# Kernel tuning notes

Measured on AMD Instinct MI355X. Metric: run time of the kernel, lower is better.

The kernel has to match this reference:

```python
import jax, jax.numpy as jnp
import numpy as np

B, TY, TX, TT, H, VS, VT = 32, 64, 64, 64, 512, 32000, 32000


def setup_inputs() -> dict:
    key = jax.random.key(0)
    ks = jax.random.split(key, 12)
    s = 0.05  # weight scale for numerical sanity
    return {
        "y_hidden": jax.random.normal(ks[0], (B, TY, H), jnp.float32),
        "y_hidden_null": jax.random.normal(ks[1], (1, H), jnp.float32),
        "target_state": jax.random.normal(ks[2], (B, TT, H), jnp.float32),
        "W_em": jax.random.normal(ks[3], (H, H), jnp.float32) * s,
        "b_em": jnp.zeros((H,), jnp.float32),
        "W_sv": jax.random.normal(ks[4], (H, VS), jnp.float32) * s,
        "b_sv": jnp.zeros((VS,), jnp.float32),
        "W_tv": jax.random.normal(ks[5], (H, VT), jnp.float32) * s,
        "b_tv": jnp.zeros((VT,), jnp.float32),
        "sources": jax.random.randint(ks[6], (B, TX), 0, VS, jnp.int32),
        "targets": jax.random.randint(ks[7], (B, TT), 0, VT, jnp.int32),
        "target_lengths": jax.random.randint(ks[8], (B,), 1, TT + 1, jnp.int32),
    }


def reference(y_hidden, y_hidden_null, target_state, W_em, b_em, W_sv, b_sv,
              W_tv, b_tv, sources, targets, target_lengths):
    # ---- emission (get_emission) ----
    ts = jnp.tanh(y_hidden @ W_em + b_em)            # (B, Ty, H)
    tsn = jnp.tanh(y_hidden_null @ W_em + b_em)      # (1, H)
    em_sm = jax.nn.softmax(ts @ W_sv + b_sv, axis=-1)        # (B, Ty, Vs)
    null_sm = jax.nn.softmax(tsn @ W_sv + b_sv, axis=-1)     # (1, Vs)
    # vectorized replacement of tf.map_fn + tf.gather: per-batch gather of source token columns
    em_g = jnp.take_along_axis(em_sm, sources[:, None, :], axis=-1)  # (B, Ty, Tx)
    null_g = null_sm[0][sources]                                     # (B, Tx)
    null_tiled = jnp.broadcast_to(null_g[:, None, :], (sources.shape[0], ts.shape[1], sources.shape[1]))
    emission_prob = jnp.concatenate([em_g, null_tiled], axis=1)      # (B, 2*Ty, Tx)

    # ---- reconstruction (get_target); keep_prob = 1 so dropout is identity ----
    tgt_sm = jax.nn.softmax(target_state @ W_tv + b_tv, axis=-1)     # (B, Tt, Vt)
    target_predicted = jnp.argmax(tgt_sm, axis=-1)                   # (B, Tt)
    # gather[t, targets[t]] then * eye then reduce_sum == diagonal pick: prob of own token
    target_prob = jnp.take_along_axis(tgt_sm, targets[:, :, None].astype(jnp.int32), axis=-1)[..., 0]  # (B, Tt)
    Tt = targets.shape[1]
    target_mask = (jnp.arange(Tt)[None, :] < target_lengths[:, None]).astype(target_prob.dtype)
    reconstruction_expectation = target_prob * target_mask
    reconstruction_expectation_log = jnp.log(target_prob) * target_mask
    return emission_prob, reconstruction_expectation, reconstruction_expectation_log, target_predicted
```

## Files before the change

### kernel.cpp

```cpp
#include <hip/hip_runtime.h>
#include <math.h>

#define H 512
#define V 32000
#define NVB 250

typedef unsigned short ushort_t;
typedef __attribute__((ext_vector_type(8))) short short8;
typedef __attribute__((ext_vector_type(4))) float f32x4;

__device__ __forceinline__ unsigned short f2bf(float x) {
    unsigned int u; __builtin_memcpy(&u, &x, 4);
    unsigned int r = (u + 0x7fffu + ((u >> 16) & 1u)) >> 16;
    return (unsigned short)r;
}
__device__ __forceinline__ float bfu2f(unsigned short h) {
    unsigned int u = ((unsigned int)h) << 16;
    float f; __builtin_memcpy(&f, &u, 4);
    return f;
}

__device__ __forceinline__ void t2_insert(float& m1, int& c1, float& m2, int& c2,
                                          float v, int idx) {
    if (v > m1 || (v == m1 && idx < c1)) { m2 = m1; c2 = c1; m1 = v; c1 = idx; }
    else if (v > m2 || (v == m2 && idx < c2)) { m2 = v; c2 = idx; }
}

__device__ __forceinline__ void gl16(const void* g, void* l) {
    __builtin_amdgcn_global_load_lds(
        (const __attribute__((address_space(1))) void*)g,
        (__attribute__((address_space(3))) void*)l,
        16, 0, 0);
}

__global__ __launch_bounds__(256) void k_emstate(
    const float* __restrict__ y_hidden, const float* __restrict__ y_null,
    const float* __restrict__ W, const float* __restrict__ bias,
    float* __restrict__ ts)
{
    const int NR = 2049;
    __shared__ float As[16][64];
    __shared__ float Bs[16][64];
    int rb = blockIdx.y, cb = blockIdx.x;
    int row0 = rb * 64, col0 = cb * 64;
    int tid = threadIdx.x;
    int tr = tid >> 4, tc = tid & 15;
    float acc[4][4] = {};
    for (int k0 = 0; k0 < H; k0 += 16) {
        {
            int r = tid >> 2;
            int kk = (tid & 3) << 2;
            int row = row0 + r;
            float4 v = make_float4(0.f, 0.f, 0.f, 0.f);
            if (row < 2048)       v = *(const float4*)&y_hidden[row * H + k0 + kk];
            else if (row == 2048) v = *(const float4*)&y_null[k0 + kk];
            As[kk + 0][r] = v.x; As[kk + 1][r] = v.y;
            As[kk + 2][r] = v.z; As[kk + 3][r] = v.w;
            int bk = tid >> 4, bc = (tid & 15) << 2;
            *(float4*)&Bs[bk][bc] = *(const float4*)&W[(k0 + bk) * H + col0 + bc];
        }
        __syncthreads();
#pragma unroll
        for (int kk = 0; kk < 16; ++kk) {
            float4 a = *(float4*)&As[kk][tr * 4];
            float4 b = *(float4*)&Bs[kk][tc * 4];
            float av[4] = {a.x, a.y, a.z, a.w};
            float bv[4] = {b.x, b.y, b.z, b.w};
#pragma unroll
            for (int i = 0; i < 4; i++)
#pragma unroll
                for (int j = 0; j < 4; j++) acc[i][j] += av[i] * bv[j];
        }
        __syncthreads();
    }
#pragma unroll
    for (int i = 0; i < 4; i++) {
        int row = row0 + tr * 4 + i;
        if (row >= NR) break;
#pragma unroll
        for (int j = 0; j < 4; j++) {
            int col = col0 + tc * 4 + j;
            ts[(size_t)row * H + col] = tanhf(acc[i][j] + bias[col]);
        }
    }
}

__global__ __launch_bounds__(256) void k_packA(
    const float* __restrict__ A, int nvalid, int nb16,
    ushort_t* __restrict__ Ph, ushort_t* __restrict__ Pl)
{
    int c = blockIdx.x * 256 + threadIdx.x;
    if (c >= nb16 * 1024) return;
    int n16 = c >> 10, rem = c & 1023, k32 = rem >> 6, l = rem & 63;
    int m = n16 * 16 + (l & 15);
    int k = k32 * 32 + (l >> 4) * 8;
    float v[8];
    if (m < nvalid) {
        *(float4*)&v[0] = *(const float4*)&A[(size_t)m * H + k];
        *(float4*)&v[4] = *(const float4*)&A[(size_t)m * H + k + 4];
    } else {
#pragma unroll
        for (int j = 0; j < 8; ++j) v[j] = 0.f;
    }
    unsigned int hh[4], lo[4];
#pragma unroll
    for (int p = 0; p < 4; ++p) {
        unsigned short h0 = f2bf(v[2 * p]), h1 = f2bf(v[2 * p + 1]);
        hh[p] = (unsigned int)h0 | ((unsigned int)h1 << 16);
        unsigned short l0 = f2bf(v[2 * p] - bfu2f(h0));
        unsigned short l1 = f2bf(v[2 * p + 1] - bfu2f(h1));
        lo[p] = (unsigned int)l0 | ((unsigned int)l1 << 16);
    }
    size_t o = ((size_t)n16 * 16 + k32) * 512 + l * 8;
    *(uint4*)&Ph[o] = make_uint4(hh[0], hh[1], hh[2], hh[3]);
    *(uint4*)&Pl[o] = make_uint4(lo[0], lo[1], lo[2], lo[3]);
}

__global__ __launch_bounds__(256) void k_packW(
    const float* __restrict__ W,
    ushort_t* __restrict__ Ph, ushort_t* __restrict__ Pl)
{
    int c = blockIdx.x * 256 + threadIdx.x;
    int n16 = c >> 10, rem = c & 1023, k32 = rem >> 6, l = rem & 63;
    int n = n16 * 16 + (l & 15);
    int k = k32 * 32 + (l >> 4) * 8;
    float v[8];
#pragma unroll
    for (int j = 0; j < 8; ++j) v[j] = W[(size_t)(k + j) * V + n];
    unsigned int hh[4], lo[4];
#pragma unroll
    for (int p = 0; p < 4; ++p) {
        unsigned short h0 = f2bf(v[2 * p]), h1 = f2bf(v[2 * p + 1]);
        hh[p] = (unsigned int)h0 | ((unsigned int)h1 << 16);
        unsigned short l0 = f2bf(v[2 * p] - bfu2f(h0));
        unsigned short l1 = f2bf(v[2 * p + 1] - bfu2f(h1));
        lo[p] = (unsigned int)l0 | ((unsigned int)l1 << 16);
    }
    size_t o = ((size_t)n16 * 16 + k32) * 512 + l * 8;
    *(uint4*)&Ph[o] = make_uint4(hh[0], hh[1], hh[2], hh[3]);
    *(uint4*)&Pl[o] = make_uint4(lo[0], lo[1], lo[2], lo[3]);
}

template<bool TOP2>
__global__ __launch_bounds__(256) void k_gemm(
    int nrb,
    const ushort_t* __restrict__ Ah, const ushort_t* __restrict__ Al,
    const ushort_t* __restrict__ Bh, const ushort_t* __restrict__ Bl,
    const float* __restrict__ bias,
    float* __restrict__ pL,
    float* __restrict__ pM1, float* __restrict__ pM2,
    int* __restrict__ pI1, int* __restrict__ pI2)
{
    const int id  = blockIdx.x;
    const int xcd = id & 7;
    const int seq = id >> 3;
    const int rbg = xcd >> 2;
    const int vbg = xcd & 3;
    const int g0  = (nrb + 1) >> 1;
    const int nrbg = rbg ? (nrb - g0) : g0;
    const int vbl = seq / nrbg;
    const int rbl = seq - vbl * nrbg;
    const int vbsz = (vbg < 2) ? 63 : 62;
    if (vbl >= vbsz) return;
    const int rb = rbg ? (g0 + rbl) : rbl;
    const int vb = vbg * 63 - ((vbg == 3) ? 1 : 0) + vbl;

    __shared__ __attribute__((aligned(16))) ushort_t AshB[2][8 * 512];
    __shared__ __attribute__((aligned(16))) ushort_t AslB[2][8 * 512];
    __shared__ __attribute__((aligned(16))) ushort_t BshB[2][8 * 512];
    __shared__ __attribute__((aligned(16))) ushort_t BslB[2][8 * 512];
    __shared__ float sc_s[128][2];
    __shared__ float sc_m1[128][2], sc_m2[128][2];
    __shared__ int   sc_c1[128][2], sc_c2[128][2];

    const int tid = threadIdx.x;
    const int row0 = rb * 128, col0 = vb * 128;
    const int lane = tid & 63, w = tid >> 6;
    const int wy = w >> 1, wx = w & 1;

    f32x4 acc[4][4];
#pragma unroll
    for (int i = 0; i < 4; ++i)
#pragma unroll
        for (int j = 0; j < 4; ++j)
#pragma unroll
            for (int r = 0; r < 4; ++r) acc[i][j][r] = 0.f;

    const ushort_t* gsrc = (w == 0) ? Ah : (w == 1) ? Al : (w == 2) ? Bh : Bl;
    ushort_t* ld0 = (w == 0) ? AshB[0] : (w == 1) ? AslB[0] : (w == 2) ? BshB[0] : BslB[0];
    ushort_t* ld1 = (w == 0) ? AshB[1] : (w == 1) ? AslB[1] : (w == 2) ? BshB[1] : BslB[1];
    const int n16base = ((w < 2) ? row0 : col0) >> 4;

#pragma unroll
    for (int mb = 0; mb < 8; ++mb)
        gl16(gsrc + (((size_t)(n16base + mb) * 16 + 0) << 9) + lane * 8,
             ld0 + mb * 512);
    __builtin_amdgcn_s_waitcnt(0x0F70);
    __builtin_amdgcn_s_barrier();

#pragma unroll 2
    for (int it = 0; it < 16; ++it) {
        const int cur = it & 1;
        const ushort_t* cAh = AshB[cur];
        const ushort_t* cAl = AslB[cur];
        const ushort_t* cBh = BshB[cur];
        const ushort_t* cBl = BslB[cur];

        short8 ahf[4], alf[4], bhf[4], blf[4];
#pragma unroll
        for (int i = 0; i < 4; ++i) {
            ahf[i] = *(const short8*)&cAh[((wy * 4 + i) << 9) + (lane << 3)];
            alf[i] = *(const short8*)&cAl[((wy * 4 + i) << 9) + (lane << 3)];
            bhf[i] = *(const short8*)&cBh[((wx * 4 + i) << 9) + (lane << 3)];
            blf[i] = *(const short8*)&cBl[((wx * 4 + i) << 9) + (lane << 3)];
        }

        if (it < 15) {
            ushort_t* nxt = cur ? ld0 : ld1;
#pragma unroll
            for (int mb = 0; mb < 8; ++mb)
                gl16(gsrc + (((size_t)(n16base + mb) * 16 + (it + 1)) << 9) + lane * 8,
                     nxt + mb * 512);
        }
        __builtin_amdgcn_sched_barrier(0);

#pragma unroll
        for (int i = 0; i < 4; ++i)
#pragma unroll
            for (int j = 0; j < 4; ++j) {
                acc[i][j] = __builtin_amdgcn_mfma_f32_16x16x32_bf16(ahf[i], bhf[j], acc[i][j], 0, 0, 0);
                acc[i][j] = __builtin_amdgcn_mfma_f32_16x16x32_bf16(ahf[i], blf[j], acc[i][j], 0, 0, 0);
                acc[i][j] = __builtin_amdgcn_mfma_f32_16x16x32_bf16(alf[i], bhf[j], acc[i][j], 0, 0, 0);
            }
        __builtin_amdgcn_sched_barrier(0);

        __builtin_amdgcn_s_waitcnt(0x0F70);
        __builtin_amdgcn_s_barrier();
    }

    float b4[4];
#pragma unroll
    for (int j = 0; j < 4; ++j) b4[j] = bias[col0 + wx * 64 + j * 16 + (lane & 15)];
    const int colbase = col0 + wx * 64 + (lane & 15);

#pragma unroll
    for (int i = 0; i < 4; ++i) {
#pragma unroll
        for (int r = 0; r < 4; ++r) {
            float s = 0.f;
            float m1 = -3e38f, m2 = -3e38f; int c1 = 0x7fffffff, c2 = 0x7fffffff;
#pragma unroll
            for (int j = 0; j < 4; ++j) {
                float v = acc[i][j][r] + b4[j];
                s += __expf(v);
                if (TOP2) t2_insert(m1, c1, m2, c2, v, colbase + j * 16);
            }
            for (int st = 1; st < 16; st <<= 1) {
                s += __shfl_xor(s, st, 64);
                if (TOP2) {
                    float om1 = __shfl_xor(m1, st, 64); int oc1 = __shfl_xor(c1, st, 64);
                    float om2 = __shfl_xor(m2, st, 64); int oc2 = __shfl_xor(c2, st, 64);
                    t2_insert(m1, c1, m2, c2, om1, oc1);
                    t2_insert(m1, c1, m2, c2, om2, oc2);
                }
            }
            if ((lane & 15) == 0) {
                int rowLoc = wy * 64 + i * 16 + (lane >> 4) * 4 + r;
                sc_s[rowLoc][wx] = s;
                if (TOP2) {
                    sc_m1[rowLoc][wx] = m1; sc_c1[rowLoc][wx] = c1;
                    sc_m2[rowLoc][wx] = m2; sc_c2[rowLoc][wx] = c2;
                }
            }
        }
    }
    __syncthreads();
    if (tid < 128) {
        int rowG = row0 + tid;
        pL[(size_t)rowG * NVB + vb] = sc_s[tid][0] + sc_s[tid][1];
        if (TOP2) {
            float m1 = sc_m1[tid][0]; int c1 = sc_c1[tid][0];
            float m2 = sc_m2[tid][0]; int c2 = sc_c2[tid][0];
            t2_insert(m1, c1, m2, c2, sc_m1[tid][1], sc_c1[tid][1]);
            t2_insert(m1, c1, m2, c2, sc_m2[tid][1], sc_c2[tid][1]);
            pM1[(size_t)rowG * NVB + vb] = m1;
            pM2[(size_t)rowG * NVB + vb] = m2;
            pI1[(size_t)rowG * NVB + vb] = c1;
            pI2[(size_t)rowG * NVB + vb] = c2;
        }
    }
}

__global__ __launch_bounds__(256) void k_combine_src(
    const float* __restrict__ pL, int nrows, float* __restrict__ L)
{
    int w = threadIdx.x >> 6, ll = threadIdx.x & 63;
    int row = blockIdx.x * 4 + w;
    if (row >= nrows) return;
    const float* p = &pL[(size_t)row * NVB];
    float s = 0.f;
    for (int vb = ll; vb < NVB; vb += 64) s += p[vb];
    for (int st = 1; st < 64; st <<= 1) s += __shfl_xor(s, st, 64);
    if (ll == 0) L[row] = s;
}

__global__ __launch_bounds__(256) void k_combine_tgt(
    const float* __restrict__ pL,
    const float* __restrict__ pM1, const float* __restrict__ pM2,
    const int* __restrict__ pI1, const int* __restrict__ pI2,
    float* __restrict__ L, int* __restrict__ C0, int* __restrict__ C1)
{
    int w = threadIdx.x >> 6, ll = threadIdx.x & 63;
    int row = blockIdx.x * 4 + w;
    if (row >= 2048) return;
    size_t base = (size_t)row * NVB;
    float s = 0.f;
    float m1 = -3e38f, m2 = -3e38f; int c1 = 0x7fffffff, c2 = 0x7fffffff;
    for (int vb = ll; vb < NVB; vb += 64) {
        s += pL[base + vb];
        t2_insert(m1, c1, m2, c2, pM1[base + vb], pI1[base + vb]);
        t2_insert(m1, c1, m2, c2, pM2[base + vb], pI2[base + vb]);
    }
    for (int st = 1; st < 64; st <<= 1) {
        s += __shfl_xor(s, st, 64);
        float om1 = __shfl_xor(m1, st, 64); int oc1 = __shfl_xor(c1, st, 64);
        float om2 = __shfl_xor(m2, st, 64); int oc2 = __shfl_xor(c2, st, 64);
        t2_insert(m1, c1, m2, c2, om1, oc1);
        t2_insert(m1, c1, m2, c2, om2, oc2);
    }
    if (ll == 0) { L[row] = s; C0[row] = c1; C1[row] = c2; }
}

__global__ __launch_bounds__(256) void k_emission(
    const float* __restrict__ ts, const float* __restrict__ W_sv,
    const float* __restrict__ b_sv, const int* __restrict__ sources,
    const float* __restrict__ L, float* __restrict__ out)
{
    __shared__ float wcol[H];
    __shared__ float sbias;
    int b = blockIdx.y, tx = blockIdx.x;
    int tid = threadIdx.x;
    int s = sources[b * 64 + tx];
    wcol[tid]       = W_sv[(size_t)tid * V + s];
    wcol[tid + 256] = W_sv[(size_t)(tid + 256) * V + s];
    if (tid == 0) sbias = b_sv[s];
    __syncthreads();
    int w = tid >> 6, ll = tid & 63;
    for (int r = w; r <= 64; r += 4) {
        int row = (r < 64) ? (b * 64 + r) : 2048;
        const float* a = &ts[(size_t)row * H];
        float sum = 0.f;
#pragma unroll
        for (int j = 0; j < 8; ++j) sum += a[ll * 8 + j] * wcol[ll * 8 + j];
        for (int m2 = 1; m2 < 64; m2 <<= 1) sum += __shfl_xor(sum, m2, 64);
        float prob = __expf(sum + sbias) / L[row];
        if (r < 64) {
            if (ll == 0) out[b * 8192 + r * 64 + tx] = prob;
        } else {
            out[b * 8192 + (64 + ll) * 64 + tx] = prob;
        }
    }
}

__global__ __launch_bounds__(256) void k_target_final(
    const float* __restrict__ tstate,
    const float* __restrict__ W_tv, const float* __restrict__ b_tv,
    const int* __restrict__ targets, const int* __restrict__ tlen,
    const float* __restrict__ L, const int* __restrict__ C0,
    const int* __restrict__ C1,
    float* __restrict__ out_exp, float* __restrict__ out_log,
    float* __restrict__ out_pred)
{
    int w = threadIdx.x >> 6, ll = threadIdx.x & 63;
    int row = blockIdx.x * 4 + w;
    if (row >= 2048) return;
    int tok = targets[row], a0 = C0[row], a1 = C1[row];
    const float* a = &tstate[(size_t)row * H];
    float s0 = 0.f, s1 = 0.f, s2 = 0.f;
#pragma unroll
    for (int j = 0; j < 8; ++j) {
        int k = ll * 8 + j;
        float av = a[k];
        const float* wr = &W_tv[(size_t)k * V];
        s0 += av * wr[tok]; s1 += av * wr[a0]; s2 += av * wr[a1];
    }
    for (int st = 1; st < 64; st <<= 1) {
        s0 += __shfl_xor(s0, st, 64);
        s1 += __shfl_xor(s1, st, 64);
        s2 += __shfl_xor(s2, st, 64);
    }
    if (ll == 0) {
        float ltok = s0 + b_tv[tok];
        float v0 = s1 + b_tv[a0], v1 = s2 + b_tv[a1];
        int pred = (v1 > v0 || (v1 == v0 && a1 < a0)) ? a1 : a0;
        float Li = L[row];
        int bb = row >> 6, t = row & 63;
        int mask = (t < tlen[bb]) ? 1 : 0;
        float prob = __expf(ltok) / Li;
        out_exp[row]  = mask ? prob : 0.f;
        out_log[row]  = mask ? (ltok - __logf(Li)) : 0.f;
        out_pred[row] = (float)pred;
    }
}

extern "C" void kernel_launch(void* const* d_in, const int* in_sizes, int n_in,
                              void* d_out, int out_size, void* d_ws, size_t ws_size,
                              hipStream_t stream)
{
    const float* y_hidden = (const float*)d_in[0];
    const float* y_null   = (const float*)d_in[1];
    const float* tstate   = (const float*)d_in[2];
    const float* W_em     = (const float*)d_in[3];
    const float* b_em     = (const float*)d_in[4];
    const float* W_sv     = (const float*)d_in[5];
    const float* b_sv     = (const float*)d_in[6];
    const float* W_tv     = (const float*)d_in[7];
    const float* b_tv     = (const float*)d_in[8];
    const int*   sources  = (const int*)d_in[9];
    const int*   targets  = (const int*)d_in[10];
    const int*   tlen     = (const int*)d_in[11];

    float* out = (float*)d_out;
    float* out_em   = out;
    float* out_exp  = out + 262144;
    float* out_log  = out + 264192;
    float* out_pred = out + 266240;

    float* ws = (float*)d_ws;
    size_t off = 0;
    float*    ts    = ws + off; off += (size_t)2176 * H;
    ushort_t* tsPh  = (ushort_t*)(ws + off); off += (size_t)2176 * H / 2;
    ushort_t* tsPl  = (ushort_t*)(ws + off); off += (size_t)2176 * H / 2;
    ushort_t* ttPh  = (ushort_t*)(ws + off); off += (size_t)2048 * H / 2;
    ushort_t* ttPl  = (ushort_t*)(ws + off); off += (size_t)2048 * H / 2;
    ushort_t* Wh    = (ushort_t*)(ws + off); off += (size_t)V * H / 2;
    ushort_t* Wl    = (ushort_t*)(ws + off); off += (size_t)V * H / 2;
    float* pL0  = ws + off; off += (size_t)2176 * NVB;
    float* pL1  = ws + off; off += (size_t)2048 * NVB;
    float* pM1a = ws + off; off += (size_t)2048 * NVB;
    float* pM1b = ws + off; off += (size_t)2048 * NVB;
    int*   pI1a = (int*)(ws + off); off += (size_t)2048 * NVB;
    int*   pI1b = (int*)(ws + off); off += (size_t)2048 * NVB;
    float* L0   = ws + off; off += 2176;
    float* L1   = ws + off; off += 2048;
    int*   C0   = (int*)(ws + off); off += 2048;
    int*   C1   = (int*)(ws + off); off += 2048;

    k_emstate<<<dim3(8, 33), 256, 0, stream>>>(y_hidden, y_null, W_em, b_em, ts);

    k_packA<<<(136 * 1024) / 256, 256, 0, stream>>>(ts, 2049, 136, tsPh, tsPl);
    k_packA<<<(128 * 1024) / 256, 256, 0, stream>>>(tstate, 2048, 128, ttPh, ttPl);

    k_packW<<<(2000 * 1024) / 256, 256, 0, stream>>>(W_sv, Wh, Wl);
    k_gemm<false><<<dim3(8 * 567), 256, 0, stream>>>(
        17, tsPh, tsPl, Wh, Wl, b_sv, pL0, nullptr, nullptr, nullptr, nullptr);

    k_packW<<<(2000 * 1024) / 256, 256, 0, stream>>>(W_tv, Wh, Wl);
    k_gemm<true><<<dim3(8 * 504), 256, 0, stream>>>(
        16, ttPh, ttPl, Wh, Wl, b_tv, pL1, pM1a, pM1b, pI1a, pI1b);

    k_combine_src<<<(2049 + 3) / 4, 256, 0, stream>>>(pL0, 2049, L0);
    k_combine_tgt<<<2048 / 4, 256, 0, stream>>>(pL1, pM1a, pM1b, pI1a, pI1b,
                                                L1, C0, C1);

    k_emission<<<dim3(64, 32), 256, 0, stream>>>(ts, W_sv, b_sv, sources, L0, out_em);

    k_target_final<<<2048 / 4, 256, 0, stream>>>(tstate, W_tv, b_tv, targets, tlen,
                                                 L1, C0, C1,
                                                 out_exp, out_log, out_pred);
}
```

Measured before the change: 1.278 ms.

## Load GEMM fragments directly from global into registers, dropping LDS staging

Replaces the LDS double-buffered global_load_lds staging in the split-bf16 GEMM with direct per-wave global loads of prepacked fragments into registers, software-pipelined two stages deep. This removes the LDS round trip and the block-wide barriers per k-step, and the kernel also asks for two blocks per CU through launch bounds. In exchange each wave fetches its own A/B fragments, so data shared between waves (A across wx, B across wy) is read from global/L2 twice. The doubled register buffers may also press against the register limit set by the occupancy hint.

```diff
diff --git a/kernel.cpp b/kernel.cpp
--- a/kernel.cpp
+++ b/kernel.cpp
@@ -24,13 +24,6 @@
                                           float v, int idx) {
     if (v > m1 || (v == m1 && idx < c1)) { m2 = m1; c2 = c1; m1 = v; c1 = idx; }
     else if (v > m2 || (v == m2 && idx < c2)) { m2 = v; c2 = idx; }
-}
-
-__device__ __forceinline__ void gl16(const void* g, void* l) {
-    __builtin_amdgcn_global_load_lds(
-        (const __attribute__((address_space(1))) void*)g,
-        (__attribute__((address_space(3))) void*)l,
-        16, 0, 0);
 }
 
 __global__ __launch_bounds__(256) void k_emstate(
@@ -142,7 +135,7 @@
 }
 
 template<bool TOP2>
-__global__ __launch_bounds__(256) void k_gemm(
+__global__ __launch_bounds__(256, 2) void k_gemm(
     int nrb,
     const ushort_t* __restrict__ Ah, const ushort_t* __restrict__ Al,
     const ushort_t* __restrict__ Bh, const ushort_t* __restrict__ Bl,
@@ -165,10 +158,6 @@
     const int rb = rbg ? (g0 + rbl) : rbl;
     const int vb = vbg * 63 - ((vbg == 3) ? 1 : 0) + vbl;
 
-    __shared__ __attribute__((aligned(16))) ushort_t AshB[2][8 * 512];
-    __shared__ __attribute__((aligned(16))) ushort_t AslB[2][8 * 512];
-    __shared__ __attribute__((aligned(16))) ushort_t BshB[2][8 * 512];
-    __shared__ __attribute__((aligned(16))) ushort_t BslB[2][8 * 512];
     __shared__ float sc_s[128][2];
     __shared__ float sc_m1[128][2], sc_m2[128][2];
     __shared__ int   sc_c1[128][2], sc_c2[128][2];
@@ -186,57 +175,48 @@
 #pragma unroll
             for (int r = 0; r < 4; ++r) acc[i][j][r] = 0.f;
 
-    const ushort_t* gsrc = (w == 0) ? Ah : (w == 1) ? Al : (w == 2) ? Bh : Bl;
-    ushort_t* ld0 = (w == 0) ? AshB[0] : (w == 1) ? AslB[0] : (w == 2) ? BshB[0] : BslB[0];
-    ushort_t* ld1 = (w == 0) ? AshB[1] : (w == 1) ? AslB[1] : (w == 2) ? BshB[1] : BslB[1];
-    const int n16base = ((w < 2) ? row0 : col0) >> 4;
-
-#pragma unroll
-    for (int mb = 0; mb < 8; ++mb)
-        gl16(gsrc + (((size_t)(n16base + mb) * 16 + 0) << 9) + lane * 8,
-             ld0 + mb * 512);
-    __builtin_amdgcn_s_waitcnt(0x0F70);
-    __builtin_amdgcn_s_barrier();
-
-#pragma unroll 2
-    for (int it = 0; it < 16; ++it) {
-        const int cur = it & 1;
-        const ushort_t* cAh = AshB[cur];
-        const ushort_t* cAl = AslB[cur];
-        const ushort_t* cBh = BshB[cur];
-        const ushort_t* cBl = BslB[cur];
-
-        short8 ahf[4], alf[4], bhf[4], blf[4];
-#pragma unroll
-        for (int i = 0; i < 4; ++i) {
-            ahf[i] = *(const short8*)&cAh[((wy * 4 + i) << 9) + (lane << 3)];
-            alf[i] = *(const short8*)&cAl[((wy * 4 + i) << 9) + (lane << 3)];
-            bhf[i] = *(const short8*)&cBh[((wx * 4 + i) << 9) + (lane << 3)];
-            blf[i] = *(const short8*)&cBl[((wx * 4 + i) << 9) + (lane << 3)];
-        }
-
-        if (it < 15) {
-            ushort_t* nxt = cur ? ld0 : ld1;
-#pragma unroll
-            for (int mb = 0; mb < 8; ++mb)
-                gl16(gsrc + (((size_t)(n16base + mb) * 16 + (it + 1)) << 9) + lane * 8,
-                     nxt + mb * 512);
-        }
-        __builtin_amdgcn_sched_barrier(0);
-
-#pragma unroll
-        for (int i = 0; i < 4; ++i)
-#pragma unroll
-            for (int j = 0; j < 4; ++j) {
-                acc[i][j] = __builtin_amdgcn_mfma_f32_16x16x32_bf16(ahf[i], bhf[j], acc[i][j], 0, 0, 0);
-                acc[i][j] = __builtin_amdgcn_mfma_f32_16x16x32_bf16(ahf[i], blf[j], acc[i][j], 0, 0, 0);
-                acc[i][j] = __builtin_amdgcn_mfma_f32_16x16x32_bf16(alf[i], bhf[j], acc[i][j], 0, 0, 0);
-            }
-        __builtin_amdgcn_sched_barrier(0);
-
-        __builtin_amdgcn_s_waitcnt(0x0F70);
-        __builtin_amdgcn_s_barrier();
-    }
+    int a_off[4], b_off[4];
+#pragma unroll
+    for (int i = 0; i < 4; ++i) {
+        a_off[i] = ((rb * 8 + wy * 4 + i) * 16) * 512 + lane * 8;
+        b_off[i] = ((vb * 8 + wx * 4 + i) * 16) * 512 + lane * 8;
+    }
+
+    short8 ah_[2][4], al_[2][4], bh_[2][4], bl_[2][4];
+
+#define LOADC(S, IT) {                                                   \
+    const int ko = (IT) * 512;                                           \
+    _Pragma("unroll")                                                    \
+    for (int i = 0; i < 4; ++i) {                                        \
+        ah_[S][i] = *(const short8*)&Ah[a_off[i] + ko];                  \
+        al_[S][i] = *(const short8*)&Al[a_off[i] + ko];                  \
+        bh_[S][i] = *(const short8*)&Bh[b_off[i] + ko];                  \
+        bl_[S][i] = *(const short8*)&Bl[b_off[i] + ko];                  \
+    } }
+
+#define MFMAS(S) {                                                       \
+    _Pragma("unroll")                                                    \
+    for (int i = 0; i < 4; ++i)                                          \
+        _Pragma("unroll")                                                \
+        for (int j = 0; j < 4; ++j) {                                    \
+            acc[i][j] = __builtin_amdgcn_mfma_f32_16x16x32_bf16(         \
+                ah_[S][i], bh_[S][j], acc[i][j], 0, 0, 0);               \
+            acc[i][j] = __builtin_amdgcn_mfma_f32_16x16x32_bf16(         \
+                ah_[S][i], bl_[S][j], acc[i][j], 0, 0, 0);               \
+            acc[i][j] = __builtin_amdgcn_mfma_f32_16x16x32_bf16(         \
+                al_[S][i], bh_[S][j], acc[i][j], 0, 0, 0);               \
+        } }
+
+    LOADC(0, 0)
+#pragma unroll 1
+    for (int it = 0; it < 16; it += 2) {
+        LOADC(1, it + 1)
+        MFMAS(0)
+        if (it + 2 < 16) LOADC(0, it + 2)
+        MFMAS(1)
+    }
+#undef LOADC
+#undef MFMAS
 
     float b4[4];
 #pragma unroll
```

New measurement: 1.329 ms. 1.04x slower.

## Single-buffer LDS tiles in GEMM and raise occupancy via launch bounds

Applied to the files above, without the earlier changes.

Removes the LDS double buffer in the split-bf16 GEMM, so each K-step loads its tile, waits, synchronizes, computes, and syncs again. LDS per block is halved, and launch_bounds(256,4) asks for four blocks per CU, so more resident waves can hide latency instead of in-block prefetch. The cost is that global-to-LDS loads no longer overlap with the MFMA work inside a block, and each iteration now has an extra barrier. The register cap from the launch bound may also cause spills.

```diff
diff --git a/kernel.cpp b/kernel.cpp
--- a/kernel.cpp
+++ b/kernel.cpp
@@ -142,7 +142,7 @@
 }
 
 template<bool TOP2>
-__global__ __launch_bounds__(256) void k_gemm(
+__global__ __launch_bounds__(256, 4) void k_gemm(
     int nrb,
     const ushort_t* __restrict__ Ah, const ushort_t* __restrict__ Al,
     const ushort_t* __restrict__ Bh, const ushort_t* __restrict__ Bl,
@@ -165,10 +165,10 @@
     const int rb = rbg ? (g0 + rbl) : rbl;
     const int vb = vbg * 63 - ((vbg == 3) ? 1 : 0) + vbl;
 
-    __shared__ __attribute__((aligned(16))) ushort_t AshB[2][8 * 512];
-    __shared__ __attribute__((aligned(16))) ushort_t AslB[2][8 * 512];
-    __shared__ __attribute__((aligned(16))) ushort_t BshB[2][8 * 512];
-    __shared__ __attribute__((aligned(16))) ushort_t BslB[2][8 * 512];
+    __shared__ __attribute__((aligned(16))) ushort_t Ash[8 * 512];
+    __shared__ __attribute__((aligned(16))) ushort_t Asl[8 * 512];
+    __shared__ __attribute__((aligned(16))) ushort_t Bsh[8 * 512];
+    __shared__ __attribute__((aligned(16))) ushort_t Bsl[8 * 512];
     __shared__ float sc_s[128][2];
     __shared__ float sc_m1[128][2], sc_m2[128][2];
     __shared__ int   sc_c1[128][2], sc_c2[128][2];
@@ -187,43 +187,27 @@
             for (int r = 0; r < 4; ++r) acc[i][j][r] = 0.f;
 
     const ushort_t* gsrc = (w == 0) ? Ah : (w == 1) ? Al : (w == 2) ? Bh : Bl;
-    ushort_t* ld0 = (w == 0) ? AshB[0] : (w == 1) ? AslB[0] : (w == 2) ? BshB[0] : BslB[0];
-    ushort_t* ld1 = (w == 0) ? AshB[1] : (w == 1) ? AslB[1] : (w == 2) ? BshB[1] : BslB[1];
+    ushort_t* ld = (w == 0) ? Ash : (w == 1) ? Asl : (w == 2) ? Bsh : Bsl;
     const int n16base = ((w < 2) ? row0 : col0) >> 4;
 
-#pragma unroll
-    for (int mb = 0; mb < 8; ++mb)
-        gl16(gsrc + (((size_t)(n16base + mb) * 16 + 0) << 9) + lane * 8,
-             ld0 + mb * 512);
-    __builtin_amdgcn_s_waitcnt(0x0F70);
-    __builtin_amdgcn_s_barrier();
-
-#pragma unroll 2
+#pragma unroll 1
     for (int it = 0; it < 16; ++it) {
-        const int cur = it & 1;
-        const ushort_t* cAh = AshB[cur];
-        const ushort_t* cAl = AslB[cur];
-        const ushort_t* cBh = BshB[cur];
-        const ushort_t* cBl = BslB[cur];
+#pragma unroll
+        for (int mb = 0; mb < 8; ++mb)
+            gl16(gsrc + (((size_t)(n16base + mb) * 16 + it) << 9) + lane * 8,
+                 ld + mb * 512);
+        __builtin_amdgcn_s_waitcnt(0x0F70);
+        __builtin_amdgcn_s_barrier();
+        __builtin_amdgcn_sched_barrier(0);
 
         short8 ahf[4], alf[4], bhf[4], blf[4];
 #pragma unroll
         for (int i = 0; i < 4; ++i) {
-            ahf[i] = *(const short8*)&cAh[((wy * 4 + i) << 9) + (lane << 3)];
-            alf[i] = *(const short8*)&cAl[((wy * 4 + i) << 9) + (lane << 3)];
-            bhf[i] = *(const short8*)&cBh[((wx * 4 + i) << 9) + (lane << 3)];
-            blf[i] = *(const short8*)&cBl[((wx * 4 + i) << 9) + (lane << 3)];
-        }
-
-        if (it < 15) {
-            ushort_t* nxt = cur ? ld0 : ld1;
-#pragma unroll
-            for (int mb = 0; mb < 8; ++mb)
-                gl16(gsrc + (((size_t)(n16base + mb) * 16 + (it + 1)) << 9) + lane * 8,
-                     nxt + mb * 512);
-        }
-        __builtin_amdgcn_sched_barrier(0);
-
+            ahf[i] = *(const short8*)&Ash[((wy * 4 + i) << 9) + (lane << 3)];
+            alf[i] = *(const short8*)&Asl[((wy * 4 + i) << 9) + (lane << 3)];
+            bhf[i] = *(const short8*)&Bsh[((wx * 4 + i) << 9) + (lane << 3)];
+            blf[i] = *(const short8*)&Bsl[((wx * 4 + i) << 9) + (lane << 3)];
+        }
 #pragma unroll
         for (int i = 0; i < 4; ++i)
 #pragma unroll
@@ -233,8 +217,6 @@
                 acc[i][j] = __builtin_amdgcn_mfma_f32_16x16x32_bf16(alf[i], bhf[j], acc[i][j], 0, 0, 0);
             }
         __builtin_amdgcn_sched_barrier(0);
-
-        __builtin_amdgcn_s_waitcnt(0x0F70);
         __builtin_amdgcn_s_barrier();
     }
 
```

Measured after the change: 1.215 ms. -4.9%, faster.
